# Performance work log

Measured on AMD Instinct MI355X. Metric: run time of the kernel, lower is better.

## Reference

```python
import jax, jax.numpy as jnp
import numpy as np

D_MODEL = 1024
D_EXPERT = 1024
NUM_EXPERTS = 8
TOP_K = 2


def setup_inputs() -> dict:
    key = jax.random.key(0)
    k_x, k_r, k1, k2, k3 = jax.random.split(key, 5)
    scale = 0.02
    x = jax.random.normal(k_x, (4, 2048, D_MODEL), dtype=jnp.float32)
    Wr = jax.random.normal(k_r, (D_MODEL, NUM_EXPERTS), dtype=jnp.float32) * scale
    # stacked per-expert SwiGLU weights (Linear with bias=False)
    W1 = jax.random.normal(k1, (NUM_EXPERTS, D_MODEL, D_EXPERT), dtype=jnp.float32) * scale
    W2 = jax.random.normal(k2, (NUM_EXPERTS, D_EXPERT, D_MODEL), dtype=jnp.float32) * scale
    W3 = jax.random.normal(k3, (NUM_EXPERTS, D_MODEL, D_EXPERT), dtype=jnp.float32) * scale
    return {"x": x, "Wr": Wr, "W1": W1, "W2": W2, "W3": W3}


def reference(x, Wr, W1, W2, W3):
    B, T, C = x.shape
    xf = x.reshape(-1, C)                       # [N, C], N = B*T
    logits = xf @ Wr                            # [N, E]
    probs = jax.nn.softmax(logits, axis=-1)
    topk_p, topk_i = jax.lax.top_k(probs, TOP_K)  # [N, K]
    topk_p = topk_p / jnp.sum(topk_p, axis=-1, keepdims=True)
    out = jnp.zeros_like(xf)
    for e in range(NUM_EXPERTS):
        # combine weight per token for this expert (0 if not routed here)
        w_e = jnp.sum(topk_p * (topk_i == e), axis=-1)  # [N]
        h = jax.nn.silu(xf @ W1[e]) * (xf @ W3[e])       # [N, d_expert]
        y = h @ W2[e]                                    # [N, C]
        out = out + w_e[:, None] * y
    return out.reshape(B, T, C)
```

## Files before the change

kernel.cpp:

```cpp
#include <hip/hip_runtime.h>
#include <hip/hip_bf16.h>

typedef __attribute__((ext_vector_type(8))) short short8;
typedef __attribute__((ext_vector_type(4))) short short4v;
typedef __attribute__((ext_vector_type(4))) unsigned short ushort4v;
typedef __attribute__((ext_vector_type(4))) float f32x4;

#define NTOK 8192
#define DM 1024
#define DE 1024
#define NE 8

__device__ __forceinline__ float bf2f(unsigned short u) {
  union { unsigned int i; float f; } v; v.i = ((unsigned int)u) << 16; return v.f;
}
__device__ __forceinline__ unsigned short f2bf(float f) {
  union { float f; unsigned int i; } v; v.f = f;
  unsigned int lsb = (v.i >> 16) & 1;
  v.i += 0x7fffu + lsb;
  return (unsigned short)(v.i >> 16);
}
__device__ __forceinline__ void gl_lds(const short* g, short* l) {
  __builtin_amdgcn_global_load_lds((const __attribute__((address_space(1))) void*)g,
                                   (__attribute__((address_space(3))) void*)l, 16, 0, 0);
}

__global__ __launch_bounds__(256) void k_prep(const float* __restrict__ W1,
                                              const float* __restrict__ W2,
                                              const float* __restrict__ W3,
                                              const float* __restrict__ x,
                                              const float* __restrict__ Wr,
                                              short* __restrict__ wcat,
                                              short* __restrict__ w2t,
                                              short* __restrict__ xb,
                                              int* __restrict__ esel,
                                              float* __restrict__ wgt) {
  const int b = blockIdx.x;
  if (b < 2048) {
    int wid = threadIdx.x >> 6, lane = threadIdx.x & 63;
    int t = b * 4 + wid;
    const float* xr = x + (size_t)t * DM;
    float acc[8];
#pragma unroll
    for (int e = 0; e < 8; e++) acc[e] = 0.f;
#pragma unroll
    for (int i = 0; i < 4; i++) {
      int kb = (i * 64 + lane) * 4;
      f32x4 v = *(const f32x4*)(xr + kb);
      ushort4v ob;
#pragma unroll
      for (int j = 0; j < 4; j++) {
        f32x4 w0 = *(const f32x4*)(Wr + (size_t)(kb + j) * 8);
        f32x4 w1 = *(const f32x4*)(Wr + (size_t)(kb + j) * 8 + 4);
        float xv = v[j];
        ob[j] = f2bf(xv);
        acc[0] += xv * w0[0]; acc[1] += xv * w0[1];
        acc[2] += xv * w0[2]; acc[3] += xv * w0[3];
        acc[4] += xv * w1[0]; acc[5] += xv * w1[1];
        acc[6] += xv * w1[2]; acc[7] += xv * w1[3];
      }
      *(ushort4v*)(xb + (size_t)t * DM + kb) = ob;
    }
#pragma unroll
    for (int off = 32; off; off >>= 1)
#pragma unroll
      for (int e = 0; e < 8; e++) acc[e] += __shfl_xor(acc[e], off);
    float m0 = -1e30f, m1 = -1e30f; int e0 = 0, e1 = 0;
#pragma unroll
    for (int e = 0; e < 8; e++) {
      float v = acc[e];
      if (v > m0) { m1 = m0; e1 = e0; m0 = v; e0 = e; }
      else if (v > m1) { m1 = v; e1 = e; }
    }
    float p = __expf(m1 - m0);
    if (lane == 0) {
      esel[2 * t] = e0; esel[2 * t + 1] = e1;
      wgt[2 * t] = 1.f / (1.f + p); wgt[2 * t + 1] = p / (1.f + p);
    }
    return;
  }
  __shared__ float t[64][65];
  const int bb = b - 2048;
  const int mid = bb >> 8;
  const int rem = bb & 255;
  const int by = rem >> 4, bx = rem & 15;
  const float* src;
  if (mid < 8)       src = W1 + (size_t)mid * (DM * DE);
  else if (mid < 16) src = W3 + (size_t)(mid - 8) * (DM * DE);
  else               src = W2 + (size_t)(mid - 16) * (DE * DM);
  int tid = threadIdx.x;
  int tr = tid >> 4, tc = tid & 15;
  int kbase = by * 64, nbase = bx * 64;
#pragma unroll
  for (int j = 0; j < 4; j++) {
    int kr = tr + j * 16;
    f32x4 v = *(const f32x4*)(src + (size_t)(kbase + kr) * 1024 + nbase + tc * 4);
    t[kr][tc * 4 + 0] = v[0]; t[kr][tc * 4 + 1] = v[1];
    t[kr][tc * 4 + 2] = v[2]; t[kr][tc * 4 + 3] = v[3];
  }
  __syncthreads();
#pragma unroll
  for (int j = 0; j < 4; j++) {
    int n = tr + j * 16;
    int ng = nbase + n;
    short4v o;
    o[0] = (short)f2bf(t[tc * 4 + 0][n]);
    o[1] = (short)f2bf(t[tc * 4 + 1][n]);
    o[2] = (short)f2bf(t[tc * 4 + 2][n]);
    o[3] = (short)f2bf(t[tc * 4 + 3][n]);
    size_t dsto;
    if (mid < 16) {
      int e = mid & 7, p = mid >> 3;
      int row_out = ((ng >> 6) * 128) + p * 64 + (ng & 63);
      dsto = (size_t)e * (2048 * 1024) + (size_t)row_out * 1024 + kbase + tc * 4;
      *(short4v*)(wcat + dsto) = o;
    } else {
      int e = mid - 16;
      dsto = (size_t)e * (1024 * 1024) + (size_t)ng * 1024 + kbase + tc * 4;
      *(short4v*)(w2t + dsto) = o;
    }
  }
}

__global__ __launch_bounds__(256) void k_rank(const int* __restrict__ esel,
                                              int* __restrict__ cnt,
                                              int* __restrict__ rank) {
  __shared__ int wcnt[4][8];
  __shared__ int woff[4][8];
  int tid = threadIdx.x;
  int lane = tid & 63, wid = tid >> 6;
  int t = blockIdx.x * 256 + tid;
  int e0 = esel[2 * t], e1 = esel[2 * t + 1];
  unsigned long long lt = (lane == 0) ? 0ull : ((~0ull) >> (64 - lane));
  int r0 = 0, r1 = 0;
#pragma unroll
  for (int e = 0; e < 8; e++) {
    unsigned long long m0 = __ballot(e0 == e);
    unsigned long long m1 = __ballot(e1 == e);
    int c0 = __popcll(m0);
    if (e0 == e) r0 = __popcll(m0 & lt);
    if (e1 == e) r1 = c0 + __popcll(m1 & lt);
    if (lane == 0) wcnt[wid][e] = c0 + __popcll(m1);
  }
  __syncthreads();
  if (tid < 8) {
    int e = tid;
    int c0 = wcnt[0][e], c1 = wcnt[1][e], c2 = wcnt[2][e], c3 = wcnt[3][e];
    int base = atomicAdd(&cnt[e], c0 + c1 + c2 + c3);
    woff[0][e] = base;
    woff[1][e] = base + c0;
    woff[2][e] = base + c0 + c1;
    woff[3][e] = base + c0 + c1 + c2;
  }
  __syncthreads();
  rank[2 * t] = woff[wid][e0] + r0;
  rank[2 * t + 1] = woff[wid][e1] + r1;
}

__global__ __launch_bounds__(256) void k_scatter(const int* __restrict__ cnt,
                                                 const int* __restrict__ esel,
                                                 const int* __restrict__ rank,
                                                 int* __restrict__ tok_of_slot,
                                                 int* __restrict__ slot_of_tok) {
  int t = blockIdx.x * 256 + threadIdx.x;
#pragma unroll
  for (int j = 0; j < 2; j++) {
    int e = esel[2 * t + j];
    int base = 0;
#pragma unroll
    for (int i = 0; i < NE; i++) base += (i < e) ? cnt[i] : 0;
    int s = base + rank[2 * t + j];
    tok_of_slot[s] = t;
    slot_of_tok[2 * t + j] = s;
  }
}

__global__ __launch_bounds__(512, 4) void k_ffn1(const short* __restrict__ Abase,
                                                 const short* __restrict__ Bbase,
                                                 const int* __restrict__ cnt,
                                                 const int* __restrict__ tok_of_slot,
                                                 short* __restrict__ outp) {
  const int NT = 16;
  const int lid = blockIdx.x;
  const int q = 32 * NT;
  const int swz = (lid & 7) * q + (lid >> 3);
  const int mt = swz & 31;
  const int pnl = swz >> 5;
  const int e = pnl / NT;
  const int nt = pnl % NT;

  const int cnt_e = cnt[e];
  const int m0 = mt * 256;
  if (m0 >= cnt_e) return;
  int bse = 0;
#pragma unroll
  for (int i = 0; i < NE; i++) bse += (i < e) ? cnt[i] : 0;
  const int n0 = nt * 128;
  const short* Bt = Bbase + (size_t)e * (2048 * 1024) + (size_t)n0 * 1024;

  __shared__ __align__(128) short Al[3][8192];
  __shared__ __align__(128) short Bl[3][4096];

  const int tid = threadIdx.x;
  const int lane = tid & 63, wid = tid >> 6;
  const int wr = wid >> 1, wcn = wid & 1;

  const short* srcA0; const short* srcA1; const short* srcB0;
  {
    int r0 = tid >> 2, c0 = (tid & 3) ^ ((r0 >> 1) & 3);
    int row0 = m0 + r0; if (row0 >= cnt_e) row0 = cnt_e - 1;
    long ar0 = (long)tok_of_slot[bse + row0];
    srcA0 = Abase + ar0 * 1024 + c0 * 8;
    int ch1 = tid + 512;
    int r1 = ch1 >> 2, c1 = (ch1 & 3) ^ ((r1 >> 1) & 3);
    int row1 = m0 + r1; if (row1 >= cnt_e) row1 = cnt_e - 1;
    long ar1 = (long)tok_of_slot[bse + row1];
    srcA1 = Abase + ar1 * 1024 + c1 * 8;
    srcB0 = Bt + (size_t)r0 * 1024 + c0 * 8;
  }
  const int lA0 = wid * 512, lA1 = wid * 512 + 4096, lB0 = wid * 512;

  int aoff[4], boff[4];
#pragma unroll
  for (int m = 0; m < 4; m++) {
    int r = wr * 64 + m * 16 + (lane & 15);
    aoff[m] = (r * 4 + ((lane >> 4) ^ ((r >> 1) & 3))) * 16;
  }
#pragma unroll
  for (int n = 0; n < 4; n++) {
    int rb = wcn * 32 + (n & 1) * 16 + (n >> 1) * 64 + (lane & 15);
    boff[n] = (rb * 4 + ((lane >> 4) ^ ((rb >> 1) & 3))) * 16;
  }

  f32x4 acc[4][4];
#pragma unroll
  for (int m = 0; m < 4; m++)
#pragma unroll
    for (int n = 0; n < 4; n++) acc[m][n] = (f32x4){0.f, 0.f, 0.f, 0.f};

#define STG_A(b, kt) { gl_lds(srcA0 + (kt) * 32, &Al[b][lA0]); \
                       gl_lds(srcA1 + (kt) * 32, &Al[b][lA1]); }
#define STG_B(b, kt) { gl_lds(srcB0 + (kt) * 32, &Bl[b][lB0]); }

  STG_A(0, 0); STG_B(0, 0);
  STG_A(1, 1); STG_B(1, 1);
  asm volatile("s_waitcnt vmcnt(3)" ::: "memory");
  __builtin_amdgcn_s_barrier();

  int cur = 0, nxt = 2;
  for (int t = 0; t < 32; ++t) {
    int ktn = (t + 2 < 32) ? (t + 2) : 31;
    const char* Ab = (const char*)Al[cur];
    const char* Bb = (const char*)Bl[cur];
    short8 a[4], b[4];
#pragma unroll
    for (int m = 0; m < 4; m++) a[m] = *(const short8*)(Ab + aoff[m]);
#pragma unroll
    for (int n = 0; n < 4; n++) b[n] = *(const short8*)(Bb + boff[n]);
    STG_A(nxt, ktn); STG_B(nxt, ktn);
    __builtin_amdgcn_s_barrier();
    __builtin_amdgcn_s_setprio(1);
#pragma unroll
    for (int m = 0; m < 4; m++)
#pragma unroll
      for (int n = 0; n < 4; n++)
        acc[m][n] = __builtin_amdgcn_mfma_f32_16x16x32_bf16(a[m], b[n], acc[m][n], 0, 0, 0);
    __builtin_amdgcn_s_setprio(0);
    asm volatile("s_waitcnt vmcnt(3)" ::: "memory");
    __builtin_amdgcn_s_barrier();
    cur = (cur == 2) ? 0 : cur + 1;
    nxt = (nxt == 2) ? 0 : nxt + 1;
  }
  asm volatile("s_waitcnt vmcnt(0)" ::: "memory");

#pragma unroll
  for (int m = 0; m < 4; m++)
#pragma unroll
    for (int cc = 0; cc < 2; cc++) {
      f32x4 v1 = acc[m][cc], v3 = acc[m][cc + 2];
      int col = nt * 64 + wcn * 32 + cc * 16 + (lane & 15);
#pragma unroll
      for (int i = 0; i < 4; i++) {
        int row = m0 + wr * 64 + m * 16 + ((lane >> 4) * 4) + i;
        if (row < cnt_e) {
          float a1v = v1[i];
          float hv = (a1v / (1.f + __expf(-a1v))) * v3[i];
          outp[(size_t)(bse + row) * DE + col] = (short)f2bf(hv);
        }
      }
    }
}

__global__ __launch_bounds__(256, 3) void k_ffn2(const short* __restrict__ Abase,
                                                 const short* __restrict__ Bbase,
                                                 const int* __restrict__ cnt,
                                                 short* __restrict__ outp) {
  const int lid = blockIdx.x;
  const int q = 512;
  const int swz = (lid & 7) * q + (lid >> 3);
  const int mt = swz & 63;
  const int pnl = swz >> 6;
  const int e = pnl >> 3;
  const int nt = pnl & 7;

  const int cnt_e = cnt[e];
  const int m0 = mt * 128;
  if (m0 >= cnt_e) return;
  int bse = 0;
#pragma unroll
  for (int i = 0; i < NE; i++) bse += (i < e) ? cnt[i] : 0;
  const int n0 = nt * 128;
  const short* Bt = Bbase + (size_t)e * (1024 * 1024) + (size_t)n0 * 1024;

  __shared__ __align__(128) short Al[3][4096];
  __shared__ __align__(128) short Bl[3][4096];

  const int tid = threadIdx.x;
  const int lane = tid & 63, wid = tid >> 6;
  const int wr = wid >> 1, wcn = wid & 1;

  const short* srcA[2]; const short* srcB[2];
#pragma unroll
  for (int i = 0; i < 2; i++) {
    int ch = tid + i * 256;
    int r = ch >> 2, c = (ch & 3) ^ ((r >> 1) & 3);
    int row = m0 + r; if (row >= cnt_e) row = cnt_e - 1;
    srcA[i] = Abase + (size_t)(bse + row) * 1024 + c * 8;
    srcB[i] = Bt + (size_t)r * 1024 + c * 8;
  }

  int aoff[4], boff[4];
#pragma unroll
  for (int m = 0; m < 4; m++) {
    int r = wr * 64 + m * 16 + (lane & 15);
    aoff[m] = (r * 4 + ((lane >> 4) ^ ((r >> 1) & 3))) * 16;
  }
#pragma unroll
  for (int n = 0; n < 4; n++) {
    int rb = wcn * 64 + n * 16 + (lane & 15);
    boff[n] = (rb * 4 + ((lane >> 4) ^ ((rb >> 1) & 3))) * 16;
  }

  f32x4 acc[4][4];
#pragma unroll
  for (int m = 0; m < 4; m++)
#pragma unroll
    for (int n = 0; n < 4; n++) acc[m][n] = (f32x4){0.f, 0.f, 0.f, 0.f};

#define STG2(b, kt) { gl_lds(srcA[0] + (kt) * 32, &Al[b][(tid + 0) * 8]); \
                      gl_lds(srcA[1] + (kt) * 32, &Al[b][(tid + 256) * 8]); \
                      gl_lds(srcB[0] + (kt) * 32, &Bl[b][(tid + 0) * 8]); \
                      gl_lds(srcB[1] + (kt) * 32, &Bl[b][(tid + 256) * 8]); }

  STG2(0, 0); STG2(1, 1);
  asm volatile("s_waitcnt vmcnt(4)" ::: "memory");
  __builtin_amdgcn_s_barrier();

  int cur = 0, nxt = 2;
  for (int t = 0; t < 32; ++t) {
    int ktn = (t + 2 < 32) ? (t + 2) : 31;
    const char* Ab = (const char*)Al[cur];
    const char* Bb = (const char*)Bl[cur];
    short8 a[4], b[4];
#pragma unroll
    for (int m = 0; m < 4; m++) a[m] = *(const short8*)(Ab + aoff[m]);
#pragma unroll
    for (int n = 0; n < 4; n++) b[n] = *(const short8*)(Bb + boff[n]);
    STG2(nxt, ktn);
    __builtin_amdgcn_s_barrier();
    __builtin_amdgcn_s_setprio(1);
#pragma unroll
    for (int m = 0; m < 4; m++)
#pragma unroll
      for (int n = 0; n < 4; n++)
        acc[m][n] = __builtin_amdgcn_mfma_f32_16x16x32_bf16(a[m], b[n], acc[m][n], 0, 0, 0);
    __builtin_amdgcn_s_setprio(0);
    asm volatile("s_waitcnt vmcnt(4)" ::: "memory");
    __builtin_amdgcn_s_barrier();
    cur = (cur == 2) ? 0 : cur + 1;
    nxt = (nxt == 2) ? 0 : nxt + 1;
  }
  asm volatile("s_waitcnt vmcnt(0)" ::: "memory");

#pragma unroll
  for (int m = 0; m < 4; m++)
#pragma unroll
    for (int n = 0; n < 4; n++) {
      f32x4 v = acc[m][n];
      int col = n0 + wcn * 64 + n * 16 + (lane & 15);
#pragma unroll
      for (int i = 0; i < 4; i++) {
        int row = m0 + wr * 64 + m * 16 + ((lane >> 4) * 4) + i;
        if (row < cnt_e)
          outp[(size_t)(bse + row) * DM + col] = (short)f2bf(v[i]);
      }
    }
}

__global__ __launch_bounds__(256) void k_combine(const short* __restrict__ y,
                                                 const int* __restrict__ slot_of_tok,
                                                 const float* __restrict__ wgt,
                                                 float* __restrict__ out) {
  int t = blockIdx.x * 2 + (threadIdx.x >> 7);
  int tt = threadIdx.x & 127;
  int s0 = slot_of_tok[2 * t], s1 = slot_of_tok[2 * t + 1];
  float w0 = wgt[2 * t], w1 = wgt[2 * t + 1];
  int c = tt * 8;
  short8 a = *(const short8*)(y + (size_t)s0 * DM + c);
  short8 b = *(const short8*)(y + (size_t)s1 * DM + c);
  f32x4 o0, o1;
#pragma unroll
  for (int j = 0; j < 4; j++) {
    o0[j] = w0 * bf2f((unsigned short)a[j]) + w1 * bf2f((unsigned short)b[j]);
    o1[j] = w0 * bf2f((unsigned short)a[j + 4]) + w1 * bf2f((unsigned short)b[j + 4]);
  }
  *(f32x4*)(out + (size_t)t * DM + c) = o0;
  *(f32x4*)(out + (size_t)t * DM + c + 4) = o1;
}

extern "C" void kernel_launch(void* const* d_in, const int* in_sizes, int n_in,
                              void* d_out, int out_size, void* d_ws, size_t ws_size,
                              hipStream_t stream) {
  const float* x  = (const float*)d_in[0];
  const float* Wr = (const float*)d_in[1];
  const float* W1 = (const float*)d_in[2];
  const float* W2 = (const float*)d_in[3];
  const float* W3 = (const float*)d_in[4];
  float* out = (float*)d_out;
  char* ws = (char*)d_ws;

  short* xb   = (short*)(ws);
  short* wcat = (short*)(ws + 16777216);
  short* w2t  = (short*)(ws + 50331648);
  short* h    = (short*)(ws + 67108864);
  short* y    = (short*)(ws + 100663296);
  char* meta = ws + 134217728;
  int* cnt          = (int*)(meta);
  int* esel         = (int*)(meta + 512);
  int* rank         = (int*)(meta + 512 + 65536);
  int* tok_of_slot  = (int*)(meta + 512 + 2 * 65536);
  int* slot_of_tok  = (int*)(meta + 512 + 3 * 65536);
  float* wgt        = (float*)(meta + 512 + 4 * 65536);

  hipMemsetAsync(cnt, 0, 32, stream);
  k_prep<<<8192, 256, 0, stream>>>(W1, W2, W3, x, Wr, wcat, w2t, xb, esel, wgt);
  k_rank<<<32, 256, 0, stream>>>(esel, cnt, rank);
  k_scatter<<<32, 256, 0, stream>>>(cnt, esel, rank, tok_of_slot, slot_of_tok);
  k_ffn1<<<dim3(32 * 8 * 16), 512, 0, stream>>>(xb, wcat, cnt, tok_of_slot, h);
  k_ffn2<<<dim3(4096), 256, 0, stream>>>(h, w2t, cnt, y);
  k_combine<<<4096, 256, 0, stream>>>(y, slot_of_tok, wgt, out);
}
```

Before: 226.6 us.

## Split FFN2 along K into two halves with 256-row tiles, reduce in combine

k_ffn2 now uses 512-thread blocks with 256-row M tiles and splits the K=1024 reduction into two halves. Each half writes bf16 partial results to a separate buffer, and the second buffer reuses the wcat workspace region. k_combine reads both partials and sums them before applying the routing weights. The aim is more parallel blocks per expert and better B-tile reuse across larger M tiles. The cost is double y-write and read traffic, bf16 rounding of the partial sums, and half as many loop iterations to hide pipeline latency.

```diff
diff --git a/kernel.cpp b/kernel.cpp
--- a/kernel.cpp
+++ b/kernel.cpp
@@ -291,43 +291,50 @@
     }
 }
 
-__global__ __launch_bounds__(256, 3) void k_ffn2(const short* __restrict__ Abase,
+__global__ __launch_bounds__(512, 2) void k_ffn2(const short* __restrict__ Abase,
                                                  const short* __restrict__ Bbase,
                                                  const int* __restrict__ cnt,
-                                                 short* __restrict__ outp) {
+                                                 short* __restrict__ y0,
+                                                 short* __restrict__ y1) {
   const int lid = blockIdx.x;
   const int q = 512;
   const int swz = (lid & 7) * q + (lid >> 3);
-  const int mt = swz & 63;
-  const int pnl = swz >> 6;
-  const int e = pnl >> 3;
-  const int nt = pnl & 7;
+  const int mt = swz & 31;
+  const int rest = swz >> 5;
+  const int kh = rest & 1;
+  const int nt = (rest >> 1) & 7;
+  const int e = rest >> 4;
 
   const int cnt_e = cnt[e];
-  const int m0 = mt * 128;
+  const int m0 = mt * 256;
   if (m0 >= cnt_e) return;
   int bse = 0;
 #pragma unroll
   for (int i = 0; i < NE; i++) bse += (i < e) ? cnt[i] : 0;
   const int n0 = nt * 128;
-  const short* Bt = Bbase + (size_t)e * (1024 * 1024) + (size_t)n0 * 1024;
-
-  __shared__ __align__(128) short Al[3][4096];
+  const int k0 = kh * 512;
+  const short* Bt = Bbase + (size_t)e * (1024 * 1024) + (size_t)n0 * 1024 + k0;
+  short* outp = kh ? y1 : y0;
+
+  __shared__ __align__(128) short Al[3][8192];
   __shared__ __align__(128) short Bl[3][4096];
 
   const int tid = threadIdx.x;
   const int lane = tid & 63, wid = tid >> 6;
   const int wr = wid >> 1, wcn = wid & 1;
 
-  const short* srcA[2]; const short* srcB[2];
-#pragma unroll
-  for (int i = 0; i < 2; i++) {
-    int ch = tid + i * 256;
-    int r = ch >> 2, c = (ch & 3) ^ ((r >> 1) & 3);
-    int row = m0 + r; if (row >= cnt_e) row = cnt_e - 1;
-    srcA[i] = Abase + (size_t)(bse + row) * 1024 + c * 8;
-    srcB[i] = Bt + (size_t)r * 1024 + c * 8;
-  }
+  const short* srcA0; const short* srcA1; const short* srcB0;
+  {
+    int r0 = tid >> 2, c0 = (tid & 3) ^ ((r0 >> 1) & 3);
+    int row0 = m0 + r0; if (row0 >= cnt_e) row0 = cnt_e - 1;
+    srcA0 = Abase + (size_t)(bse + row0) * 1024 + k0 + c0 * 8;
+    int ch1 = tid + 512;
+    int r1 = ch1 >> 2, c1 = (ch1 & 3) ^ ((r1 >> 1) & 3);
+    int row1 = m0 + r1; if (row1 >= cnt_e) row1 = cnt_e - 1;
+    srcA1 = Abase + (size_t)(bse + row1) * 1024 + k0 + c1 * 8;
+    srcB0 = Bt + (size_t)r0 * 1024 + c0 * 8;
+  }
+  const int lA0 = wid * 512, lA1 = wid * 512 + 4096, lB0 = wid * 512;
 
   int aoff[4], boff[4];
 #pragma unroll
@@ -347,18 +354,18 @@
 #pragma unroll
     for (int n = 0; n < 4; n++) acc[m][n] = (f32x4){0.f, 0.f, 0.f, 0.f};
 
-#define STG2(b, kt) { gl_lds(srcA[0] + (kt) * 32, &Al[b][(tid + 0) * 8]); \
-                      gl_lds(srcA[1] + (kt) * 32, &Al[b][(tid + 256) * 8]); \
-                      gl_lds(srcB[0] + (kt) * 32, &Bl[b][(tid + 0) * 8]); \
-                      gl_lds(srcB[1] + (kt) * 32, &Bl[b][(tid + 256) * 8]); }
-
-  STG2(0, 0); STG2(1, 1);
-  asm volatile("s_waitcnt vmcnt(4)" ::: "memory");
+#define STG2_A(b, kt) { gl_lds(srcA0 + (kt) * 32, &Al[b][lA0]); \
+                        gl_lds(srcA1 + (kt) * 32, &Al[b][lA1]); }
+#define STG2_B(b, kt) { gl_lds(srcB0 + (kt) * 32, &Bl[b][lB0]); }
+
+  STG2_A(0, 0); STG2_B(0, 0);
+  STG2_A(1, 1); STG2_B(1, 1);
+  asm volatile("s_waitcnt vmcnt(3)" ::: "memory");
   __builtin_amdgcn_s_barrier();
 
   int cur = 0, nxt = 2;
-  for (int t = 0; t < 32; ++t) {
-    int ktn = (t + 2 < 32) ? (t + 2) : 31;
+  for (int t = 0; t < 16; ++t) {
+    int ktn = (t + 2 < 16) ? (t + 2) : 15;
     const char* Ab = (const char*)Al[cur];
     const char* Bb = (const char*)Bl[cur];
     short8 a[4], b[4];
@@ -366,7 +373,7 @@
     for (int m = 0; m < 4; m++) a[m] = *(const short8*)(Ab + aoff[m]);
 #pragma unroll
     for (int n = 0; n < 4; n++) b[n] = *(const short8*)(Bb + boff[n]);
-    STG2(nxt, ktn);
+    STG2_A(nxt, ktn); STG2_B(nxt, ktn);
     __builtin_amdgcn_s_barrier();
     __builtin_amdgcn_s_setprio(1);
 #pragma unroll
@@ -375,7 +382,7 @@
       for (int n = 0; n < 4; n++)
         acc[m][n] = __builtin_amdgcn_mfma_f32_16x16x32_bf16(a[m], b[n], acc[m][n], 0, 0, 0);
     __builtin_amdgcn_s_setprio(0);
-    asm volatile("s_waitcnt vmcnt(4)" ::: "memory");
+    asm volatile("s_waitcnt vmcnt(3)" ::: "memory");
     __builtin_amdgcn_s_barrier();
     cur = (cur == 2) ? 0 : cur + 1;
     nxt = (nxt == 2) ? 0 : nxt + 1;
@@ -397,7 +404,8 @@
     }
 }
 
-__global__ __launch_bounds__(256) void k_combine(const short* __restrict__ y,
+__global__ __launch_bounds__(256) void k_combine(const short* __restrict__ y0,
+                                                 const short* __restrict__ y1,
                                                  const int* __restrict__ slot_of_tok,
                                                  const float* __restrict__ wgt,
                                                  float* __restrict__ out) {
@@ -406,13 +414,17 @@
   int s0 = slot_of_tok[2 * t], s1 = slot_of_tok[2 * t + 1];
   float w0 = wgt[2 * t], w1 = wgt[2 * t + 1];
   int c = tt * 8;
-  short8 a = *(const short8*)(y + (size_t)s0 * DM + c);
-  short8 b = *(const short8*)(y + (size_t)s1 * DM + c);
+  short8 a0 = *(const short8*)(y0 + (size_t)s0 * DM + c);
+  short8 a1 = *(const short8*)(y1 + (size_t)s0 * DM + c);
+  short8 b0 = *(const short8*)(y0 + (size_t)s1 * DM + c);
+  short8 b1 = *(const short8*)(y1 + (size_t)s1 * DM + c);
   f32x4 o0, o1;
 #pragma unroll
   for (int j = 0; j < 4; j++) {
-    o0[j] = w0 * bf2f((unsigned short)a[j]) + w1 * bf2f((unsigned short)b[j]);
-    o1[j] = w0 * bf2f((unsigned short)a[j + 4]) + w1 * bf2f((unsigned short)b[j + 4]);
+    o0[j] = w0 * (bf2f((unsigned short)a0[j]) + bf2f((unsigned short)a1[j]))
+          + w1 * (bf2f((unsigned short)b0[j]) + bf2f((unsigned short)b1[j]));
+    o1[j] = w0 * (bf2f((unsigned short)a0[j + 4]) + bf2f((unsigned short)a1[j + 4]))
+          + w1 * (bf2f((unsigned short)b0[j + 4]) + bf2f((unsigned short)b1[j + 4]));
   }
   *(f32x4*)(out + (size_t)t * DM + c) = o0;
   *(f32x4*)(out + (size_t)t * DM + c + 4) = o1;
@@ -433,7 +445,8 @@
   short* wcat = (short*)(ws + 16777216);
   short* w2t  = (short*)(ws + 50331648);
   short* h    = (short*)(ws + 67108864);
-  short* y    = (short*)(ws + 100663296);
+  short* y0   = (short*)(ws + 100663296);
+  short* y1   = wcat;
   char* meta = ws + 134217728;
   int* cnt          = (int*)(meta);
   int* esel         = (int*)(meta + 512);
@@ -447,6 +460,6 @@
   k_rank<<<32, 256, 0, stream>>>(esel, cnt, rank);
   k_scatter<<<32, 256, 0, stream>>>(cnt, esel, rank, tok_of_slot, slot_of_tok);
   k_ffn1<<<dim3(32 * 8 * 16), 512, 0, stream>>>(xb, wcat, cnt, tok_of_slot, h);
-  k_ffn2<<<dim3(4096), 256, 0, stream>>>(h, w2t, cnt, y);
-  k_combine<<<4096, 256, 0, stream>>>(y, slot_of_tok, wgt, out);
-}
+  k_ffn2<<<dim3(4096), 512, 0, stream>>>(h, w2t, cnt, y0, y1);
+  k_combine<<<4096, 256, 0, stream>>>(y0, y1, slot_of_tok, wgt, out);
+}
```

Result: slower. 254.4 us (+12.2%).
